# Performance work log

Hardware: AMD Instinct MI355X
Metric: run time of the kernel (lower is better)

The kernel has to match this reference:

```python
import jax, jax.numpy as jnp
import numpy as np

B, N, D, H, C = 4, 1024, 768, 12, 3
Dh = D // H                      # 64
HID = int(D * 4.0 * (2.0 / 3.0)) # 2048 (SwiGLU hidden)
EPS = 1e-5


def layernorm(x, g, b):
    m = jnp.mean(x, axis=-1, keepdims=True)
    v = jnp.mean(jnp.square(x - m), axis=-1, keepdims=True)
    return (x - m) * jax.lax.rsqrt(v + EPS) * g + b


def setup_inputs() -> dict:
    key = jax.random.key(0)
    ks = jax.random.split(key, 8)
    x = jax.random.normal(ks[0], (B, N, D), jnp.float32)
    coords = jax.random.uniform(ks[1], (B, N, C), jnp.float32)
    qkv_w = jax.random.normal(ks[2], (3 * D, D), jnp.float32) * 0.02
    qkv_b = jnp.zeros((3 * D,), jnp.float32)
    rel_w = jax.random.normal(ks[3], (H, C), jnp.float32) * 0.1
    ln1_g = jnp.ones((D,), jnp.float32)
    ln1_b = jnp.zeros((D,), jnp.float32)
    ln2_g = jnp.ones((D,), jnp.float32)
    ln2_b = jnp.zeros((D,), jnp.float32)
    win_w = jax.random.normal(ks[4], (2 * HID, D), jnp.float32) * 0.02
    win_b = jnp.zeros((2 * HID,), jnp.float32)
    wout_w = jax.random.normal(ks[5], (D, HID), jnp.float32) * 0.02
    wout_b = jnp.zeros((D,), jnp.float32)
    return dict(x=x, coords=coords, ln1_g=ln1_g, ln1_b=ln1_b, qkv_w=qkv_w,
                qkv_b=qkv_b, rel_w=rel_w, ln2_g=ln2_g, ln2_b=ln2_b,
                win_w=win_w, win_b=win_b, wout_w=wout_w, wout_b=wout_b)


def reference(x, coords, ln1_g, ln1_b, qkv_w, qkv_b, rel_w, ln2_g, ln2_b,
              win_w, win_b, wout_w, wout_b):
    # --- PatchAttention on norm1(x) ---
    h = layernorm(x, ln1_g, ln1_b)
    qkv = h @ qkv_w.T + qkv_b                    # (B,N,3D)
    q, k, v = jnp.split(qkv, 3, axis=-1)

    def heads(t):  # (B,N,D) -> (B,H,N,Dh)
        return t.reshape(B, N, H, Dh).transpose(0, 2, 1, 3)

    qh, kh, vh = heads(q), heads(k), heads(v)
    scale = 1.0 / np.sqrt(Dh).astype(np.float32)
    scores = jnp.einsum('bhid,bhjd->bhij', qh, kh) * scale
    # coord bias: (coords_i - coords_j) . W_h  ==  p[b,h,i] - p[b,h,j]
    p = jnp.einsum('bnc,hc->bhn', coords, rel_w)  # (B,H,N)
    scores = scores + p[:, :, :, None] - p[:, :, None, :]
    attn = jax.nn.softmax(scores, axis=-1)
    o = jnp.einsum('bhij,bhjd->bhid', attn, vh)   # (B,H,N,Dh)
    o = o.transpose(0, 2, 1, 3).reshape(B, N, D)
    x = x + o

    # --- SwiGLU FFN on norm2(x) ---
    h2 = layernorm(x, ln2_g, ln2_b)
    uv = h2 @ win_w.T + win_b                     # (B,N,2*HID)
    u, g = jnp.split(uv, 2, axis=-1)
    act = jax.nn.silu(u) * g
    return x + act @ wout_w.T + wout_b
```

## Files before the change

kernel.cpp:

```cpp
#include <hip/hip_runtime.h>
#include <math.h>

typedef unsigned short u16;
typedef __bf16 bf16x8 __attribute__((ext_vector_type(8)));
typedef __bf16 bf16x4 __attribute__((ext_vector_type(4)));
typedef u16 u16x4 __attribute__((ext_vector_type(4)));
typedef float f32x4 __attribute__((ext_vector_type(4)));

#define NTOK 1024
#define DMODEL 768
#define NHEAD 12
#define LD3 2304
#define HIDDIM 2048

__device__ __forceinline__ float b2f(u16 u) {
  unsigned int t = ((unsigned int)u) << 16;
  float f;
  __builtin_memcpy(&f, &t, 4);
  return f;
}
__device__ __forceinline__ u16 f2b(float f) {
  unsigned int t;
  __builtin_memcpy(&t, &f, 4);
  t += 0x7fffu + ((t >> 16) & 1u);
  return (u16)(t >> 16);
}

__device__ __forceinline__ void gl_lds16(const u16* g, u16* l) {
  __builtin_amdgcn_global_load_lds(
      (__attribute__((address_space(1))) const unsigned int*)g,
      (__attribute__((address_space(3))) unsigned int*)l, 16, 0, 0);
}

__global__ __launch_bounds__(256) void signal_kernel(float* __restrict__ out,
                                                     int n, float c) {
  int i = blockIdx.x * 256 + threadIdx.x;
  if (i < n) out[i] = c;
}

struct CanonJobs {
  const void* s[13];
  u16* d[13];
  int n[13];
};

__global__ __launch_bounds__(256) void canon_kernel(CanonJobs jobs) {
  __shared__ int csh;
  u16 v = ((const u16*)jobs.s[0])[2 * threadIdx.x];
  int e = (v >> 7) & 0xFF;
  unsigned long long m = __ballot(e >= 0xC0);
  if (threadIdx.x == 0) csh = 0;
  __syncthreads();
  if ((threadIdx.x & 63) == 0) atomicAdd(&csh, __popcll(m));
  __syncthreads();
  bool isf32 = csh >= 8;

  int j = blockIdx.y;
  int n4 = jobs.n[j] >> 2;
  const void* s = jobs.s[j];
  u16* d = jobs.d[j];
  for (int i = blockIdx.x * 256 + threadIdx.x; i < n4; i += gridDim.x * 256) {
    if (isf32) {
      f32x4 vv = *((const f32x4*)s + i);
      u16x4 o = {f2b(vv[0]), f2b(vv[1]), f2b(vv[2]), f2b(vv[3])};
      *((u16x4*)d + i) = o;
    } else {
      *((u16x4*)d + i) = *((const u16x4*)s + i);
    }
  }
}

__global__ __launch_bounds__(256) void ln_bf16_kernel(
    const u16* __restrict__ x, const u16* __restrict__ g,
    const u16* __restrict__ b, u16* __restrict__ out) {
  int row = blockIdx.x;
  int tid = threadIdx.x;
  const u16* xr = x + (size_t)row * DMODEL;
  float v0 = b2f(xr[tid]), v1 = b2f(xr[tid + 256]), v2 = b2f(xr[tid + 512]);
  float s = v0 + v1 + v2;
  float q = v0 * v0 + v1 * v1 + v2 * v2;
#pragma unroll
  for (int off = 32; off; off >>= 1) {
    s += __shfl_xor(s, off, 64);
    q += __shfl_xor(q, off, 64);
  }
  __shared__ float rs[4], rq[4];
  int wv = tid >> 6;
  if ((tid & 63) == 0) { rs[wv] = s; rq[wv] = q; }
  __syncthreads();
  s = rs[0] + rs[1] + rs[2] + rs[3];
  q = rq[0] + rq[1] + rq[2] + rq[3];
  float mean = s * (1.0f / 768.0f);
  float var = q * (1.0f / 768.0f) - mean * mean;
  float inv = rsqrtf(var + 1e-5f);
  u16* outr = out + (size_t)row * DMODEL;
  outr[tid]       = f2b((v0 - mean) * inv * b2f(g[tid])       + b2f(b[tid]));
  outr[tid + 256] = f2b((v1 - mean) * inv * b2f(g[tid + 256]) + b2f(b[tid + 256]));
  outr[tid + 512] = f2b((v2 - mean) * inv * b2f(g[tid + 512]) + b2f(b[tid + 512]));
}

__global__ __launch_bounds__(256) void ln_f32_kernel(
    const float* __restrict__ x, const u16* __restrict__ g,
    const u16* __restrict__ b, u16* __restrict__ out) {
  int row = blockIdx.x;
  int tid = threadIdx.x;
  const float* xr = x + (size_t)row * DMODEL;
  float v0 = xr[tid], v1 = xr[tid + 256], v2 = xr[tid + 512];
  float s = v0 + v1 + v2;
  float q = v0 * v0 + v1 * v1 + v2 * v2;
#pragma unroll
  for (int off = 32; off; off >>= 1) {
    s += __shfl_xor(s, off, 64);
    q += __shfl_xor(q, off, 64);
  }
  __shared__ float rs[4], rq[4];
  int wv = tid >> 6;
  if ((tid & 63) == 0) { rs[wv] = s; rq[wv] = q; }
  __syncthreads();
  s = rs[0] + rs[1] + rs[2] + rs[3];
  q = rq[0] + rq[1] + rq[2] + rq[3];
  float mean = s * (1.0f / 768.0f);
  float var = q * (1.0f / 768.0f) - mean * mean;
  float inv = rsqrtf(var + 1e-5f);
  u16* outr = out + (size_t)row * DMODEL;
  outr[tid]       = f2b((v0 - mean) * inv * b2f(g[tid])       + b2f(b[tid]));
  outr[tid + 256] = f2b((v1 - mean) * inv * b2f(g[tid + 256]) + b2f(b[tid + 256]));
  outr[tid + 512] = f2b((v2 - mean) * inv * b2f(g[tid + 512]) + b2f(b[tid + 512]));
}

__global__ __launch_bounds__(256) void gemm_bt(
    const u16* __restrict__ Ap, const u16* __restrict__ Wp,
    const u16* __restrict__ bias, u16* __restrict__ Cp, int Nn, int K) {
  __shared__ __align__(16) u16 Al[3 * 128 * 32], Bl[3 * 64 * 32];
  int lane = threadIdx.x & 63;
  int wv = threadIdx.x >> 6;
  int q16 = lane & 15, quad = lane >> 4;
  int mB0 = blockIdx.y * 128;
  int nB0 = blockIdx.x * 64;
  int mW = (wv >> 1) * 64, nW = (wv & 1) * 32;
  int srow = lane >> 2;
  int scol = ((lane & 3) ^ ((lane >> 3) & 3)) * 8;
  int sx8 = (quad ^ ((q16 >> 1) & 3)) * 8;
  int r0 = wv * 32 + srow, r1 = r0 + 16;
  int rb = wv * 16 + srow;
  const u16* Ag0 = Ap + (size_t)(mB0 + r0) * K + scol;
  const u16* Ag1 = Ap + (size_t)(mB0 + r1) * K + scol;
  const u16* Wg  = Wp + (size_t)(nB0 + rb) * K + scol;
  int ch0 = wv * 1024, ch1 = ch0 + 512, chb = wv * 512;
  int nsteps = K >> 5;
  f32x4 acc[4][2] = {};
#pragma unroll
  for (int tt = 0; tt < 2; ++tt) {
    int k0 = tt * 32;
    gl_lds16(Ag0 + k0, Al + tt * 4096 + ch0);
    gl_lds16(Ag1 + k0, Al + tt * 4096 + ch1);
    gl_lds16(Wg + k0, Bl + tt * 2048 + chb);
  }
  int n3 = nsteps / 3;
  for (int kb = 0; kb < n3; ++kb) {
#pragma unroll
    for (int c = 0; c < 3; ++c) {
      int t = kb * 3 + c;
      if (t < nsteps - 1) asm volatile("s_waitcnt vmcnt(3)" ::: "memory");
      else                asm volatile("s_waitcnt vmcnt(0)" ::: "memory");
      __builtin_amdgcn_sched_barrier(0);
      __builtin_amdgcn_s_barrier();
      __builtin_amdgcn_sched_barrier(0);
      if (t < nsteps - 2) {
        int k0 = (t + 2) * 32;
        int bs = (c + 2) % 3;
        gl_lds16(Ag0 + k0, Al + bs * 4096 + ch0);
        gl_lds16(Ag1 + k0, Al + bs * 4096 + ch1);
        gl_lds16(Wg + k0, Bl + bs * 2048 + chb);
      }
      const __bf16* Ab = (const __bf16*)(Al + c * 4096);
      const __bf16* Bb = (const __bf16*)(Bl + c * 2048);
      bf16x8 af[4], bfr[2];
#pragma unroll
      for (int si = 0; si < 4; ++si)
        af[si] = *(const bf16x8*)(Ab + (mW + si * 16 + q16) * 32 + sx8);
#pragma unroll
      for (int sj = 0; sj < 2; ++sj)
        bfr[sj] = *(const bf16x8*)(Bb + (nW + sj * 16 + q16) * 32 + sx8);
#pragma unroll
      for (int si = 0; si < 4; ++si)
#pragma unroll
        for (int sj = 0; sj < 2; ++sj)
          acc[si][sj] = __builtin_amdgcn_mfma_f32_16x16x32_bf16(af[si], bfr[sj], acc[si][sj], 0, 0, 0);
    }
  }
#pragma unroll
  for (int si = 0; si < 4; ++si)
#pragma unroll
    for (int sj = 0; sj < 2; ++sj) {
      int col = nB0 + nW + sj * 16 + q16;
      float bcol = b2f(bias[col]);
#pragma unroll
      for (int r = 0; r < 4; ++r) {
        int rowi = mB0 + mW + si * 16 + quad * 4 + r;
        Cp[(size_t)rowi * Nn + col] = f2b(acc[si][sj][r] + bcol);
      }
    }
}

__global__ __launch_bounds__(256) void gemm_out_f32(
    const u16* __restrict__ Ap, const u16* __restrict__ Wp,
    const u16* __restrict__ bias, const float* __restrict__ res,
    float* __restrict__ out) {
  __shared__ __align__(16) u16 Al[2 * 4096], Bl[2 * 4096];
  int lane = threadIdx.x & 63;
  int wv = threadIdx.x >> 6;
  int q16 = lane & 15, quad = lane >> 4;
  int mB0 = blockIdx.y * 64;
  int nB0 = blockIdx.x * 64;
  int mW = (wv >> 1) * 32, nW = (wv & 1) * 32;
  int lr = lane >> 3, ls = lane & 7;
  int sg = (ls ^ lr) * 8;
  int sx0 = (quad ^ (q16 & 7)) * 8;
  int sx1 = ((4 | quad) ^ (q16 & 7)) * 8;
  const u16* Ag = Ap + (size_t)(mB0 + wv * 16 + lr) * 2048 + sg;
  const u16* Wg = Wp + (size_t)(nB0 + wv * 16 + lr) * 2048 + sg;
  int ch = wv * 1024;
  f32x4 acc[2][2] = {};
#pragma unroll
  for (int i = 0; i < 2; ++i) {
    gl_lds16(Ag + (size_t)i * 8 * 2048, Al + ch + i * 512);
    gl_lds16(Wg + (size_t)i * 8 * 2048, Bl + ch + i * 512);
  }
  for (int kb = 0; kb < 16; ++kb) {
#pragma unroll
    for (int c = 0; c < 2; ++c) {
      int t = kb * 2 + c;
      asm volatile("s_waitcnt vmcnt(0)" ::: "memory");
      __builtin_amdgcn_sched_barrier(0);
      __builtin_amdgcn_s_barrier();
      __builtin_amdgcn_sched_barrier(0);
      if (t < 31) {
        int k0 = (t + 1) * 64;
        int bs = c ^ 1;
#pragma unroll
        for (int i = 0; i < 2; ++i) {
          gl_lds16(Ag + (size_t)i * 8 * 2048 + k0, Al + bs * 4096 + ch + i * 512);
          gl_lds16(Wg + (size_t)i * 8 * 2048 + k0, Bl + bs * 4096 + ch + i * 512);
        }
      }
      const __bf16* Ab = (const __bf16*)(Al + c * 4096);
      const __bf16* Bb = (const __bf16*)(Bl + c * 4096);
      bf16x8 a0[2], a1[2], b0[2], b1[2];
#pragma unroll
      for (int si = 0; si < 2; ++si) {
        a0[si] = *(const bf16x8*)(Ab + (mW + si * 16 + q16) * 64 + sx0);
        a1[si] = *(const bf16x8*)(Ab + (mW + si * 16 + q16) * 64 + sx1);
      }
#pragma unroll
      for (int sj = 0; sj < 2; ++sj) {
        b0[sj] = *(const bf16x8*)(Bb + (nW + sj * 16 + q16) * 64 + sx0);
        b1[sj] = *(const bf16x8*)(Bb + (nW + sj * 16 + q16) * 64 + sx1);
      }
#pragma unroll
      for (int si = 0; si < 2; ++si)
#pragma unroll
        for (int sj = 0; sj < 2; ++sj) {
          acc[si][sj] = __builtin_amdgcn_mfma_f32_16x16x32_bf16(a0[si], b0[sj], acc[si][sj], 0, 0, 0);
          acc[si][sj] = __builtin_amdgcn_mfma_f32_16x16x32_bf16(a1[si], b1[sj], acc[si][sj], 0, 0, 0);
        }
    }
  }
#pragma unroll
  for (int si = 0; si < 2; ++si)
#pragma unroll
    for (int sj = 0; sj < 2; ++sj) {
      int col = nB0 + nW + sj * 16 + q16;
      float bcol = b2f(bias[col]);
#pragma unroll
      for (int r = 0; r < 4; ++r) {
        int rowi = mB0 + mW + si * 16 + quad * 4 + r;
        size_t idx = (size_t)rowi * 768 + col;
        out[idx] = acc[si][sj][r] + bcol + res[idx];
      }
    }
}

__global__ __launch_bounds__(256) void ffn_in_kernel(
    const u16* __restrict__ hp, const u16* __restrict__ Wp,
    const u16* __restrict__ bias, u16* __restrict__ actp) {
  __shared__ __align__(16) u16 Al[2 * 8192], Bl[2 * 4096];
  int lane = threadIdx.x & 63;
  int wv = threadIdx.x >> 6;
  int q16 = lane & 15, quad = lane >> 4;
  int mB0 = blockIdx.y * 128;
  int cB0 = blockIdx.x * 32;
  int mW = (wv >> 1) * 64;
  int cW = (wv & 1) * 16;
  int lr = lane >> 3, ls = lane & 7;
  int sg = (ls ^ lr) * 8;
  int sx0 = (quad ^ (q16 & 7)) * 8;
  int sx1 = ((4 | quad) ^ (q16 & 7)) * 8;
  const u16* Ag = hp + (size_t)(mB0 + wv * 32 + lr) * DMODEL + sg;
  int rB0 = wv * 16 + lr, rB1 = rB0 + 8;
  int gb0 = (rB0 < 32) ? (cB0 + rB0) : (HIDDIM + cB0 + rB0 - 32);
  int gb1 = (rB1 < 32) ? (cB0 + rB1) : (HIDDIM + cB0 + rB1 - 32);
  const u16* Wg0 = Wp + (size_t)gb0 * DMODEL + sg;
  const u16* Wg1 = Wp + (size_t)gb1 * DMODEL + sg;
  int chA = wv * 2048, chB = wv * 1024;
  f32x4 au[4] = {}, ag[4] = {};
#pragma unroll
  for (int i = 0; i < 4; ++i)
    gl_lds16(Ag + (size_t)i * 8 * DMODEL, Al + chA + i * 512);
  gl_lds16(Wg0, Bl + chB);
  gl_lds16(Wg1, Bl + chB + 512);
  for (int kb = 0; kb < 6; ++kb) {
#pragma unroll
    for (int c = 0; c < 2; ++c) {
      int t = kb * 2 + c;
      asm volatile("s_waitcnt vmcnt(0)" ::: "memory");
      __builtin_amdgcn_sched_barrier(0);
      __builtin_amdgcn_s_barrier();
      __builtin_amdgcn_sched_barrier(0);
      if (t < 11) {
        int k0 = (t + 1) * 64;
        int bs = c ^ 1;
#pragma unroll
        for (int i = 0; i < 4; ++i)
          gl_lds16(Ag + (size_t)i * 8 * DMODEL + k0, Al + bs * 8192 + chA + i * 512);
        gl_lds16(Wg0 + k0, Bl + bs * 4096 + chB);
        gl_lds16(Wg1 + k0, Bl + bs * 4096 + chB + 512);
      }
      const __bf16* Ab = (const __bf16*)(Al + c * 8192);
      const __bf16* Bb = (const __bf16*)(Bl + c * 4096);
      bf16x8 a0[4], a1[4];
#pragma unroll
      for (int si = 0; si < 4; ++si) {
        a0[si] = *(const bf16x8*)(Ab + (mW + si * 16 + q16) * 64 + sx0);
        a1[si] = *(const bf16x8*)(Ab + (mW + si * 16 + q16) * 64 + sx1);
      }
      bf16x8 wu0 = *(const bf16x8*)(Bb + (cW + q16) * 64 + sx0);
      bf16x8 wu1 = *(const bf16x8*)(Bb + (cW + q16) * 64 + sx1);
      bf16x8 wg0 = *(const bf16x8*)(Bb + (32 + cW + q16) * 64 + sx0);
      bf16x8 wg1 = *(const bf16x8*)(Bb + (32 + cW + q16) * 64 + sx1);
#pragma unroll
      for (int si = 0; si < 4; ++si) {
        au[si] = __builtin_amdgcn_mfma_f32_16x16x32_bf16(a0[si], wu0, au[si], 0, 0, 0);
        ag[si] = __builtin_amdgcn_mfma_f32_16x16x32_bf16(a0[si], wg0, ag[si], 0, 0, 0);
      }
#pragma unroll
      for (int si = 0; si < 4; ++si) {
        au[si] = __builtin_amdgcn_mfma_f32_16x16x32_bf16(a1[si], wu1, au[si], 0, 0, 0);
        ag[si] = __builtin_amdgcn_mfma_f32_16x16x32_bf16(a1[si], wg1, ag[si], 0, 0, 0);
      }
    }
  }
  int col = cB0 + cW + q16;
  float bu = b2f(bias[col]);
  float bg = b2f(bias[HIDDIM + col]);
#pragma unroll
  for (int si = 0; si < 4; ++si) {
#pragma unroll
    for (int r = 0; r < 4; ++r) {
      int rowi = mB0 + mW + si * 16 + quad * 4 + r;
      float u = au[si][r] + bu;
      float g = ag[si][r] + bg;
      float s = u / (1.0f + __expf(-u));
      actp[(size_t)rowi * HIDDIM + col] = f2b(s * g);
    }
  }
}

__global__ __launch_bounds__(256) void vt_kernel(const u16* __restrict__ qkvp,
                                                 u16* __restrict__ vtp,
                                                 const u16* __restrict__ coords,
                                                 const u16* __restrict__ relw,
                                                 float* __restrict__ p) {
  int blk = blockIdx.x;
  int b = blk / 192;
  int rem = blk % 192;
  int h = rem >> 4;
  int nt = rem & 15;
  int wv = threadIdx.x >> 6;
  int d = threadIdx.x & 63;
  int n0 = nt * 64 + wv * 16;
  const u16* src = qkvp + ((size_t)(b * NTOK) + n0) * LD3 + 2 * DMODEL + h * 64 + d;
  u16* dst = vtp + ((size_t)((b * NHEAD + h) * 64 + d)) * NTOK + n0;
#pragma unroll
  for (int c = 0; c < 2; ++c) {
    u16 buf[8] __attribute__((aligned(16)));
#pragma unroll
    for (int i = 0; i < 8; ++i) buf[i] = src[(size_t)(c * 8 + i) * LD3];
    *(uint4*)(dst + c * 8) = *(const uint4*)buf;
  }
  if (nt == 0) {
    const float LOG2E = 1.4426950408889634f;
    float w0 = b2f(relw[h * 3 + 0]), w1 = b2f(relw[h * 3 + 1]), w2 = b2f(relw[h * 3 + 2]);
    float* prow = p + (size_t)(b * NHEAD + h) * NTOK;
    for (int n = threadIdx.x; n < NTOK; n += 256) {
      int idx = b * NTOK + n;
      float c0 = b2f(coords[idx * 3 + 0]);
      float c1 = b2f(coords[idx * 3 + 1]);
      float c2 = b2f(coords[idx * 3 + 2]);
      prow[n] = (c0 * w0 + c1 * w1 + c2 * w2) * LOG2E;
    }
  }
}

__global__ __launch_bounds__(256) void attn_kernel(
    const u16* __restrict__ qkvp, const u16* __restrict__ vtp,
    const float* __restrict__ p2, const u16* __restrict__ xp,
    float* __restrict__ x1) {
  const __bf16* qb = (const __bf16*)qkvp;
  __shared__ __align__(16) u16 Kl[4][32 * 64];
  __shared__ __align__(16) u16 Vl[4][64 * 32];
  __shared__ __align__(16) u16 Pl[4][16][40];
  __shared__ __align__(16) float Pb[1024];
  int lane = threadIdx.x & 63;
  int wv = threadIdx.x >> 6;
  int hw = blockIdx.x;
  int g = hw % 48;
  int nt = hw / 48;
  int b = g / 12, h = g % 12;
  int i0 = (nt * 4 + wv) * 16;
  int q16 = lane & 15, quad = lane >> 4;

  const float scl2 = 0.125f * 1.4426950408889634f;

  const __bf16* qrow = qb + ((size_t)(b * NTOK) + i0 + q16) * LD3 + h * 64;
  bf16x8 bq0 = *(const bf16x8*)(qrow + quad * 8);
  bf16x8 bq1 = *(const bf16x8*)(qrow + 32 + quad * 8);

  const float* prow = p2 + (size_t)(b * NHEAD + h) * NTOK;

  int krw = wv * 8 + (lane >> 3);
  int ks  = (lane & 7) ^ (krw & 7);
  const u16* kg0 = qkvp + (size_t)(b * NTOK) * LD3 + DMODEL + h * 64 + ks * 8;
  int vrw = wv * 16 + (lane >> 2);
  int vs  = (lane & 3) ^ ((vrw >> 1) & 3);
  const u16* vg0 = vtp + ((size_t)((b * NHEAD + h) * 64 + vrw)) * NTOK + vs * 8;

  int kx0 = (quad ^ (q16 & 7)) << 3;
  int kx1 = ((4 | quad) ^ (q16 & 7)) << 3;
  int vx  = (quad ^ ((q16 >> 1) & 3)) << 3;

  float mrun = -1e30f, lsum = 0.f;
  f32x4 accO[4] = {};

  gl_lds16((const u16*)(prow + wv * 256 + lane * 4), (u16*)&Pb[wv * 256]);
#pragma unroll
  for (int tt = 0; tt < 3; ++tt) {
    gl_lds16(kg0 + (size_t)(tt * 32 + krw) * LD3, &Kl[tt][wv * 512]);
    gl_lds16(vg0 + tt * 32, &Vl[tt][wv * 512]);
  }

  for (int kb = 0; kb < 8; ++kb) {
#pragma unroll
    for (int c = 0; c < 4; ++c) {
      int t = kb * 4 + c;
      if (t < 30)       asm volatile("s_waitcnt vmcnt(4)" ::: "memory");
      else if (t == 30) asm volatile("s_waitcnt vmcnt(2)" ::: "memory");
      else              asm volatile("s_waitcnt vmcnt(0)" ::: "memory");
      __builtin_amdgcn_sched_barrier(0);
      __builtin_amdgcn_s_barrier();
      __builtin_amdgcn_sched_barrier(0);
      if (t < 29) {
        int j = (t + 3) * 32;
        gl_lds16(kg0 + (size_t)(j + krw) * LD3, &Kl[(c + 3) & 3][wv * 512]);
        gl_lds16(vg0 + j, &Vl[(c + 3) & 3][wv * 512]);
      }

      int j0 = t * 32;
      const __bf16* Kb = (const __bf16*)Kl[c];
      bf16x8 ka00 = *(const bf16x8*)(Kb + q16 * 64 + kx0);
      bf16x8 ka01 = *(const bf16x8*)(Kb + q16 * 64 + kx1);
      bf16x8 ka10 = *(const bf16x8*)(Kb + (16 + q16) * 64 + kx0);
      bf16x8 ka11 = *(const bf16x8*)(Kb + (16 + q16) * 64 + kx1);
      f32x4 st0 = {}, st1 = {};
      st0 = __builtin_amdgcn_mfma_f32_16x16x32_bf16(ka00, bq0, st0, 0, 0, 0);
      st0 = __builtin_amdgcn_mfma_f32_16x16x32_bf16(ka01, bq1, st0, 0, 0, 0);
      st1 = __builtin_amdgcn_mfma_f32_16x16x32_bf16(ka10, bq0, st1, 0, 0, 0);
      st1 = __builtin_amdgcn_mfma_f32_16x16x32_bf16(ka11, bq1, st1, 0, 0, 0);

      f32x4 pjl = *(const f32x4*)(&Pb[j0 + 4 * quad]);
      f32x4 pjh = *(const f32x4*)(&Pb[j0 + 16 + 4 * quad]);
      float sl[4], sh[4];
#pragma unroll
      for (int r = 0; r < 4; ++r) {
        sl[r] = st0[r] * scl2 - pjl[r];
        sh[r] = st1[r] * scl2 - pjh[r];
      }
      float lm = fmaxf(fmaxf(fmaxf(sl[0], sl[1]), fmaxf(sl[2], sl[3])),
                       fmaxf(fmaxf(sh[0], sh[1]), fmaxf(sh[2], sh[3])));
      lm = fmaxf(lm, __shfl_xor(lm, 16, 64));
      lm = fmaxf(lm, __shfl_xor(lm, 32, 64));
      float mn = fmaxf(mrun, lm);
      float alpha = exp2f(mrun - mn);
      mrun = mn;
      float pl[4], ph[4];
#pragma unroll
      for (int r = 0; r < 4; ++r) {
        pl[r] = exp2f(sl[r] - mn);
        ph[r] = exp2f(sh[r] - mn);
      }
      float ts = (pl[0] + pl[1]) + (pl[2] + pl[3]) +
                 (ph[0] + ph[1]) + (ph[2] + ph[3]);
      ts += __shfl_xor(ts, 16, 64);
      ts += __shfl_xor(ts, 32, 64);
      lsum = lsum * alpha + ts;

      bf16x4 w0 = {(__bf16)pl[0], (__bf16)pl[1], (__bf16)pl[2], (__bf16)pl[3]};
      bf16x4 w1 = {(__bf16)ph[0], (__bf16)ph[1], (__bf16)ph[2], (__bf16)ph[3]};
      *(bf16x4*)(&Pl[wv][q16][4 * quad]) = w0;
      *(bf16x4*)(&Pl[wv][q16][16 + 4 * quad]) = w1;
      bf16x8 ap = *(const bf16x8*)(&Pl[wv][q16][quad * 8]);

      const __bf16* Vb = (const __bf16*)Vl[c];
#pragma unroll
      for (int ds = 0; ds < 4; ++ds) {
        bf16x8 av = *(const bf16x8*)(Vb + (ds * 16 + q16) * 32 + vx);
        f32x4 cc = accO[ds];
#pragma unroll
        for (int r = 0; r < 4; ++r) cc[r] *= alpha;
        accO[ds] = __builtin_amdgcn_mfma_f32_16x16x32_bf16(av, ap, cc, 0, 0, 0);
      }
    }
  }

  float rl = 1.0f / lsum;
  size_t rowbase = ((size_t)(b * NTOK) + i0 + q16) * DMODEL + h * 64;
#pragma unroll
  for (int ds = 0; ds < 4; ++ds) {
    int d0 = ds * 16 + quad * 4;
    u16x4 xv = *(const u16x4*)(xp + rowbase + d0);
    f32x4 ov;
#pragma unroll
    for (int r = 0; r < 4; ++r) ov[r] = b2f(xv[r]) + accO[ds][r] * rl;
    *(f32x4*)(x1 + rowbase + d0) = ov;
  }
}

extern "C" void kernel_launch(void* const* d_in, const int* in_sizes, int n_in,
                              void* d_out, int out_size, void* d_ws, size_t ws_size,
                              hipStream_t stream) {
  static const int esz[13] = {3145728, 12288, 768, 768, 1769472, 2304, 36,
                              768, 768, 3145728, 4096, 1572864, 768};
  float sig = -1.f;
  if (n_in != 13) {
    sig = 6000.f + 100.f * (float)n_in;
  } else {
    for (int i = 0; i < 13; ++i)
      if (in_sizes[i] != esz[i]) { sig = 1000.f + 100.f * (float)i; break; }
  }
  if (sig < 0.f && ws_size < 57258496ULL) sig = 3000.f;
  if (sig < 0.f && out_size != 3145728) sig = 3100.f;
  if (sig >= 0.f) {
    signal_kernel<<<(out_size + 255) / 256, 256, 0, stream>>>((float*)d_out, out_size, sig);
    return;
  }

  char* ws = (char*)d_ws;
  u16*  cx      = (u16*)(ws + 256);
  u16*  cqkvw   = (u16*)(ws + 6291712);
  u16*  cwinw   = (u16*)(ws + 9830656);
  u16*  cwoutw  = (u16*)(ws + 16122112);
  u16*  ccoords = (u16*)(ws + 19267840);
  u16*  cln1g   = (u16*)(ws + 19292416);
  u16*  cln1b   = (u16*)(ws + 19293952);
  u16*  cqkvb   = (u16*)(ws + 19295488);
  u16*  crelw   = (u16*)(ws + 19300096);
  u16*  cln2g   = (u16*)(ws + 19300352);
  u16*  cln2b   = (u16*)(ws + 19301888);
  u16*  cwinb   = (u16*)(ws + 19303424);
  u16*  cwoutb  = (u16*)(ws + 19311616);
  u16*  h       = (u16*)(ws + 19313152);
  u16*  qkv     = (u16*)(ws + 25604608);
  float* pbuf   = (float*)(ws + 44478976);
  float* x1     = (float*)(ws + 44675584);
  u16*  act     = qkv;
  u16*  vt      = h;

  CanonJobs jobs;
  u16* dsts[13] = {cx, ccoords, cln1g, cln1b, cqkvw, cqkvb, crelw,
                   cln2g, cln2b, cwinw, cwinb, cwoutw, cwoutb};
  for (int i = 0; i < 13; ++i) {
    jobs.s[i] = d_in[i];
    jobs.d[i] = dsts[i];
    jobs.n[i] = in_sizes[i];
  }
  canon_kernel<<<dim3(768, 13), 256, 0, stream>>>(jobs);

  ln_bf16_kernel<<<4096, 256, 0, stream>>>(cx, cln1g, cln1b, h);
  gemm_bt<<<dim3(36, 32), 256, 0, stream>>>(h, cqkvw, cqkvb, qkv, 2304, 768);
  vt_kernel<<<768, 256, 0, stream>>>(qkv, vt, ccoords, crelw, pbuf);
  attn_kernel<<<768, 256, 0, stream>>>(qkv, vt, pbuf, cx, x1);
  ln_f32_kernel<<<4096, 256, 0, stream>>>(x1, cln2g, cln2b, h);
  ffn_in_kernel<<<dim3(64, 32), 256, 0, stream>>>(h, cwinw, cwinb, act);
  gemm_out_f32<<<dim3(12, 64), 256, 0, stream>>>(act, cwoutw, cwoutb, x1,
                                                 (float*)d_out);
}
```

Measured before the change: 268.8 us.

## Use 64-key tiles with double buffering in attention kernel

The attention kernel now processes 64 keys per iteration instead of 32, with a 2-stage double buffer replacing the 4-stage, 3-ahead prefetch pipeline. This halves the number of barriers and online-softmax rescale steps and doubles the MFMA work per step. In exchange, every iteration waits for vmcnt(0), so only one tile is in flight and there is less latency hiding. The P and V tiles get a new XOR-swizzled layout to match.

```diff
diff --git a/kernel.cpp b/kernel.cpp
--- a/kernel.cpp
+++ b/kernel.cpp
@@ -407,9 +407,9 @@
     const float* __restrict__ p2, const u16* __restrict__ xp,
     float* __restrict__ x1) {
   const __bf16* qb = (const __bf16*)qkvp;
-  __shared__ __align__(16) u16 Kl[4][32 * 64];
-  __shared__ __align__(16) u16 Vl[4][64 * 32];
-  __shared__ __align__(16) u16 Pl[4][16][40];
+  __shared__ __align__(16) u16 Kl[2][64 * 64];
+  __shared__ __align__(16) u16 Vl[2][64 * 64];
+  __shared__ __align__(16) u16 Pl[4][16][64];
   __shared__ __align__(16) float Pb[1024];
   int lane = threadIdx.x & 63;
   int wv = threadIdx.x >> 6;
@@ -428,97 +428,104 @@
 
   const float* prow = p2 + (size_t)(b * NHEAD + h) * NTOK;
 
-  int krw = wv * 8 + (lane >> 3);
-  int ks  = (lane & 7) ^ (krw & 7);
-  const u16* kg0 = qkvp + (size_t)(b * NTOK) * LD3 + DMODEL + h * 64 + ks * 8;
-  int vrw = wv * 16 + (lane >> 2);
-  int vs  = (lane & 3) ^ ((vrw >> 1) & 3);
-  const u16* vg0 = vtp + ((size_t)((b * NHEAD + h) * 64 + vrw)) * NTOK + vs * 8;
+  int lr = lane >> 3, ls = lane & 7;
+  int krw = wv * 16 + lr;
+  int ksl = ls ^ (krw & 7);
+  const u16* kg0 = qkvp + (size_t)(b * NTOK) * LD3 + DMODEL + h * 64 + ksl * 8;
+  const u16* vg0 = vtp + ((size_t)((b * NHEAD + h) * 64 + krw)) * NTOK + ksl * 8;
 
   int kx0 = (quad ^ (q16 & 7)) << 3;
   int kx1 = ((4 | quad) ^ (q16 & 7)) << 3;
-  int vx  = (quad ^ ((q16 >> 1) & 3)) << 3;
 
   float mrun = -1e30f, lsum = 0.f;
   f32x4 accO[4] = {};
 
   gl_lds16((const u16*)(prow + wv * 256 + lane * 4), (u16*)&Pb[wv * 256]);
-#pragma unroll
-  for (int tt = 0; tt < 3; ++tt) {
-    gl_lds16(kg0 + (size_t)(tt * 32 + krw) * LD3, &Kl[tt][wv * 512]);
-    gl_lds16(vg0 + tt * 32, &Vl[tt][wv * 512]);
-  }
-
-  for (int kb = 0; kb < 8; ++kb) {
-#pragma unroll
-    for (int c = 0; c < 4; ++c) {
-      int t = kb * 4 + c;
-      if (t < 30)       asm volatile("s_waitcnt vmcnt(4)" ::: "memory");
-      else if (t == 30) asm volatile("s_waitcnt vmcnt(2)" ::: "memory");
-      else              asm volatile("s_waitcnt vmcnt(0)" ::: "memory");
-      __builtin_amdgcn_sched_barrier(0);
-      __builtin_amdgcn_s_barrier();
-      __builtin_amdgcn_sched_barrier(0);
-      if (t < 29) {
-        int j = (t + 3) * 32;
-        gl_lds16(kg0 + (size_t)(j + krw) * LD3, &Kl[(c + 3) & 3][wv * 512]);
-        gl_lds16(vg0 + j, &Vl[(c + 3) & 3][wv * 512]);
-      }
-
-      int j0 = t * 32;
-      const __bf16* Kb = (const __bf16*)Kl[c];
-      bf16x8 ka00 = *(const bf16x8*)(Kb + q16 * 64 + kx0);
-      bf16x8 ka01 = *(const bf16x8*)(Kb + q16 * 64 + kx1);
-      bf16x8 ka10 = *(const bf16x8*)(Kb + (16 + q16) * 64 + kx0);
-      bf16x8 ka11 = *(const bf16x8*)(Kb + (16 + q16) * 64 + kx1);
-      f32x4 st0 = {}, st1 = {};
-      st0 = __builtin_amdgcn_mfma_f32_16x16x32_bf16(ka00, bq0, st0, 0, 0, 0);
-      st0 = __builtin_amdgcn_mfma_f32_16x16x32_bf16(ka01, bq1, st0, 0, 0, 0);
-      st1 = __builtin_amdgcn_mfma_f32_16x16x32_bf16(ka10, bq0, st1, 0, 0, 0);
-      st1 = __builtin_amdgcn_mfma_f32_16x16x32_bf16(ka11, bq1, st1, 0, 0, 0);
-
-      f32x4 pjl = *(const f32x4*)(&Pb[j0 + 4 * quad]);
-      f32x4 pjh = *(const f32x4*)(&Pb[j0 + 16 + 4 * quad]);
-      float sl[4], sh[4];
-#pragma unroll
-      for (int r = 0; r < 4; ++r) {
-        sl[r] = st0[r] * scl2 - pjl[r];
-        sh[r] = st1[r] * scl2 - pjh[r];
-      }
-      float lm = fmaxf(fmaxf(fmaxf(sl[0], sl[1]), fmaxf(sl[2], sl[3])),
-                       fmaxf(fmaxf(sh[0], sh[1]), fmaxf(sh[2], sh[3])));
-      lm = fmaxf(lm, __shfl_xor(lm, 16, 64));
-      lm = fmaxf(lm, __shfl_xor(lm, 32, 64));
-      float mn = fmaxf(mrun, lm);
-      float alpha = exp2f(mrun - mn);
-      mrun = mn;
-      float pl[4], ph[4];
-#pragma unroll
-      for (int r = 0; r < 4; ++r) {
-        pl[r] = exp2f(sl[r] - mn);
-        ph[r] = exp2f(sh[r] - mn);
-      }
-      float ts = (pl[0] + pl[1]) + (pl[2] + pl[3]) +
-                 (ph[0] + ph[1]) + (ph[2] + ph[3]);
-      ts += __shfl_xor(ts, 16, 64);
-      ts += __shfl_xor(ts, 32, 64);
-      lsum = lsum * alpha + ts;
-
-      bf16x4 w0 = {(__bf16)pl[0], (__bf16)pl[1], (__bf16)pl[2], (__bf16)pl[3]};
-      bf16x4 w1 = {(__bf16)ph[0], (__bf16)ph[1], (__bf16)ph[2], (__bf16)ph[3]};
-      *(bf16x4*)(&Pl[wv][q16][4 * quad]) = w0;
-      *(bf16x4*)(&Pl[wv][q16][16 + 4 * quad]) = w1;
-      bf16x8 ap = *(const bf16x8*)(&Pl[wv][q16][quad * 8]);
-
-      const __bf16* Vb = (const __bf16*)Vl[c];
-#pragma unroll
-      for (int ds = 0; ds < 4; ++ds) {
-        bf16x8 av = *(const bf16x8*)(Vb + (ds * 16 + q16) * 32 + vx);
-        f32x4 cc = accO[ds];
-#pragma unroll
-        for (int r = 0; r < 4; ++r) cc[r] *= alpha;
-        accO[ds] = __builtin_amdgcn_mfma_f32_16x16x32_bf16(av, ap, cc, 0, 0, 0);
-      }
+  gl_lds16(kg0 + (size_t)krw * LD3, &Kl[0][wv * 1024]);
+  gl_lds16(kg0 + (size_t)(krw + 8) * LD3, &Kl[0][wv * 1024 + 512]);
+  gl_lds16(vg0, &Vl[0][wv * 1024]);
+  gl_lds16(vg0 + (size_t)8 * NTOK, &Vl[0][wv * 1024 + 512]);
+
+  for (int t = 0; t < 16; ++t) {
+    asm volatile("s_waitcnt vmcnt(0)" ::: "memory");
+    __builtin_amdgcn_sched_barrier(0);
+    __builtin_amdgcn_s_barrier();
+    __builtin_amdgcn_sched_barrier(0);
+    int c = t & 1;
+    if (t < 15) {
+      int j = (t + 1) * 64;
+      int bs = c ^ 1;
+      gl_lds16(kg0 + (size_t)(j + krw) * LD3, &Kl[bs][wv * 1024]);
+      gl_lds16(kg0 + (size_t)(j + krw + 8) * LD3, &Kl[bs][wv * 1024 + 512]);
+      gl_lds16(vg0 + j, &Vl[bs][wv * 1024]);
+      gl_lds16(vg0 + (size_t)8 * NTOK + j, &Vl[bs][wv * 1024 + 512]);
+    }
+
+    int j0 = t * 64;
+    const __bf16* Kb = (const __bf16*)Kl[c];
+    const __bf16* Vb = (const __bf16*)Vl[c];
+
+    f32x4 st[4];
+#pragma unroll
+    for (int tt = 0; tt < 4; ++tt) {
+      bf16x8 ka0 = *(const bf16x8*)(Kb + (tt * 16 + q16) * 64 + kx0);
+      bf16x8 ka1 = *(const bf16x8*)(Kb + (tt * 16 + q16) * 64 + kx1);
+      f32x4 z = {};
+      z = __builtin_amdgcn_mfma_f32_16x16x32_bf16(ka0, bq0, z, 0, 0, 0);
+      z = __builtin_amdgcn_mfma_f32_16x16x32_bf16(ka1, bq1, z, 0, 0, 0);
+      st[tt] = z;
+    }
+
+    float sv[4][4];
+#pragma unroll
+    for (int tt = 0; tt < 4; ++tt) {
+      f32x4 pj = *(const f32x4*)(&Pb[j0 + tt * 16 + 4 * quad]);
+#pragma unroll
+      for (int r = 0; r < 4; ++r) sv[tt][r] = st[tt][r] * scl2 - pj[r];
+    }
+    float lm = sv[0][0];
+#pragma unroll
+    for (int tt = 0; tt < 4; ++tt)
+#pragma unroll
+      for (int r = 0; r < 4; ++r) lm = fmaxf(lm, sv[tt][r]);
+    lm = fmaxf(lm, __shfl_xor(lm, 16, 64));
+    lm = fmaxf(lm, __shfl_xor(lm, 32, 64));
+    float mn = fmaxf(mrun, lm);
+    float alpha = exp2f(mrun - mn);
+    mrun = mn;
+    float pp[4][4];
+    float ts = 0.f;
+#pragma unroll
+    for (int tt = 0; tt < 4; ++tt) {
+      float s0 = exp2f(sv[tt][0] - mn), s1 = exp2f(sv[tt][1] - mn);
+      float s2 = exp2f(sv[tt][2] - mn), s3 = exp2f(sv[tt][3] - mn);
+      pp[tt][0] = s0; pp[tt][1] = s1; pp[tt][2] = s2; pp[tt][3] = s3;
+      ts += (s0 + s1) + (s2 + s3);
+    }
+    ts += __shfl_xor(ts, 16, 64);
+    ts += __shfl_xor(ts, 32, 64);
+    lsum = lsum * alpha + ts;
+
+#pragma unroll
+    for (int tt = 0; tt < 4; ++tt) {
+      bf16x4 w = {(__bf16)pp[tt][0], (__bf16)pp[tt][1],
+                  (__bf16)pp[tt][2], (__bf16)pp[tt][3]};
+      int wslot = (2 * tt + (quad >> 1)) ^ (q16 & 7);
+      *(bf16x4*)(&Pl[wv][q16][wslot * 8 + (quad & 1) * 4]) = w;
+    }
+    bf16x8 ap0 = *(const bf16x8*)(&Pl[wv][q16][kx0]);
+    bf16x8 ap1 = *(const bf16x8*)(&Pl[wv][q16][kx1]);
+
+#pragma unroll
+    for (int ds = 0; ds < 4; ++ds) {
+      bf16x8 av0 = *(const bf16x8*)(Vb + (ds * 16 + q16) * 64 + kx0);
+      bf16x8 av1 = *(const bf16x8*)(Vb + (ds * 16 + q16) * 64 + kx1);
+      f32x4 cc = accO[ds];
+#pragma unroll
+      for (int r = 0; r < 4; ++r) cc[r] *= alpha;
+      cc = __builtin_amdgcn_mfma_f32_16x16x32_bf16(av0, ap0, cc, 0, 0, 0);
+      cc = __builtin_amdgcn_mfma_f32_16x16x32_bf16(av1, ap1, cc, 0, 0, 0);
+      accO[ds] = cc;
     }
   }
 
```

Result: no change. 265.4 us (-1.3%).
